# Kernel tuning notes

Measured on AMD Instinct MI355X. Metric: run time of the kernel, lower is better.

The kernel has to match this reference:

```python
import jax, jax.numpy as jnp
import numpy as np

NUM_RANGES = 31   # bins [0,1)...[29,30) plus [30, inf) -> max_height=30
EPS = 1e-06
ALPHA = 0.5
NAN_VALUE = -1.0


def setup_inputs() -> dict:
    key = jax.random.key(0)
    k1, k2 = jax.random.split(key)
    shape = (64, 512, 512)
    # targets in log1p space; natural heights expm1(target) span [0, ~34)
    target = jax.random.uniform(k1, shape, dtype=jnp.float32) * 3.55
    pred = target + 0.1 * jax.random.normal(k2, shape, dtype=jnp.float32)
    return {"pred": pred, "target": target}


def reference(pred, target):
    valid = target != NAN_VALUE                      # no-data mask
    natural = jnp.expm1(target)                      # heights in natural space
    # arithmetic bin index: ranges [i, i+1) for i<30, last bin [30, inf)
    bin_idx = jnp.clip(jnp.floor(natural), 0.0, NUM_RANGES - 1).astype(jnp.int32)
    in_range = natural >= 0.0                        # samples below 0 fall in no range

    # histogram of valid, in-range samples (scatter-add)
    counts = jnp.zeros(NUM_RANGES, jnp.float32).at[bin_idx.ravel()].add(
        (valid & in_range).ravel().astype(jnp.float32))
    total_valid = jnp.sum(valid).astype(jnp.float32)
    denom = jnp.maximum(total_valid, 1.0)
    freq = counts / denom
    w = 1.0 / (freq ** ALPHA + EPS)                  # inverse-frequency weights, [31]

    base = jnp.abs(pred - target)                    # L1 in log1p space
    sample_w = jnp.where(in_range, w[bin_idx], 0.0)  # gather per-sample weight
    weighted = base * sample_w
    # mean over valid samples (out-of-range valid samples contribute 0, as in torch)
    mean_loss = jnp.sum(jnp.where(valid, weighted, 0.0)) / denom
    return mean_loss
```

## Files before the change

kernel.cpp:

```cpp
#include <hip/hip_runtime.h>
#include <math.h>

#define NBINS 31
#define NSLOT 32
#define NCOPIES 256
#define BLOCK 256
#define GRID 512
#define DEPTH 4

#define CNT_SHIFT 24
#define SUM_MASK  0xFFFFFFu
#define FIX_SCALE 32768.0f

typedef float f4 __attribute__((ext_vector_type(4)));


__device__ __forceinline__ void prep(float p, float t, unsigned hbase,
                                     unsigned& addr, unsigned& pk, unsigned& nvalid)
{
    nvalid += (t != -1.0f) ? 1u : 0u;
    bool ok = (t >= 0.0f);
    float nat = __expf(t) - 1.0f;
    unsigned b = (unsigned)(int)fminf(nat, 30.0f);
    unsigned pkv = (1u << CNT_SHIFT)
                 | (unsigned)(fabsf(p - t) * FIX_SCALE + 0.5f);
    pk   = ok ? pkv : 0u;
    addr = hbase + ((ok ? b : 31u) << 10);
}

__device__ __forceinline__ void packet(f4 p, f4 t, unsigned hbase,
                                       unsigned& nvalid)
{
    unsigned a0, a1, a2, a3, k0, k1, k2, k3;
    prep(p.x, t.x, hbase, a0, k0, nvalid);
    prep(p.y, t.y, hbase, a1, k1, nvalid);
    prep(p.z, t.z, hbase, a2, k2, nvalid);
    prep(p.w, t.w, hbase, a3, k3, nvalid);

    unsigned r0, r1, r2, r3;
    asm volatile(
        "ds_read_b32 %0, %4\n\t"
        "ds_read_b32 %1, %5\n\t"
        "ds_read_b32 %2, %6\n\t"
        "ds_read_b32 %3, %7"
        : "=&v"(r0), "=&v"(r1), "=&v"(r2), "=&v"(r3)
        : "v"(a0), "v"(a1), "v"(a2), "v"(a3));

    unsigned s0 = k0;
    unsigned s1 = k1 + (a1 == a0 ? s0 : 0u);
    unsigned s2 = k2 + (a2 == a1 ? s1 : (a2 == a0 ? s0 : 0u));
    unsigned s3 = k3 + (a3 == a2 ? s2 : (a3 == a1 ? s1 : (a3 == a0 ? s0 : 0u)));

    asm volatile(
        "s_waitcnt lgkmcnt(0)\n\t"
        "v_add_u32 %0, %0, %4\n\t"
        "v_add_u32 %1, %1, %5\n\t"
        "v_add_u32 %2, %2, %6\n\t"
        "v_add_u32 %3, %3, %7\n\t"
        "ds_write_b32 %8, %0\n\t"
        "ds_write_b32 %9, %1\n\t"
        "ds_write_b32 %10, %2\n\t"
        "ds_write_b32 %11, %3"
        : "+v"(r0), "+v"(r1), "+v"(r2), "+v"(r3)
        : "v"(s0), "v"(s1), "v"(s2), "v"(s3),
          "v"(a0), "v"(a1), "v"(a2), "v"(a3));
}

__device__ __forceinline__ void stage(unsigned* dst, const f4* p4, const f4* t4,
                                      int idx)
{
    __builtin_amdgcn_global_load_lds(
        (const __attribute__((address_space(1))) unsigned*)(const void*)(p4 + idx),
        (__attribute__((address_space(3))) unsigned*)dst, 16, 0, 0);
    __builtin_amdgcn_global_load_lds(
        (const __attribute__((address_space(1))) unsigned*)(const void*)(t4 + idx),
        (__attribute__((address_space(3))) unsigned*)(dst + 256), 16, 0, 0);
}

__device__ __forceinline__ void unstage(unsigned sa, f4& pv, f4& tv)
{
    asm volatile(
        "ds_read_b128 %0, %2\n\t"
        "ds_read_b128 %1, %2 offset:1024\n\t"
        "s_waitcnt lgkmcnt(0)"
        : "=&v"(pv), "=&v"(tv)
        : "v"(sa));
}

__global__ __launch_bounds__(BLOCK) void zero_ws_kernel(unsigned* ws)
{
    int t = threadIdx.x;
    if (t < 192) ws[t] = 0u;
}

__global__ __launch_bounds__(BLOCK, 2) void hist_kernel(
    const float* __restrict__ pred, const float* __restrict__ target, int n,
    float* __restrict__ g_sums, unsigned* __restrict__ g_cnts,
    unsigned* __restrict__ g_total)
{
    __shared__ unsigned s_hist[NSLOT * NCOPIES];
    __shared__ unsigned s_stage[BLOCK / 64][DEPTH][512];
    __shared__ float    p_sum[NBINS * 8];
    __shared__ unsigned p_cnt[NBINS * 8];
    __shared__ unsigned s_tot[BLOCK / 64];

    const int tid = threadIdx.x;
    {
        uint4 z = make_uint4(0u, 0u, 0u, 0u);
        uint4* h4 = (uint4*)s_hist;
        #pragma unroll
        for (int k = 0; k < (NSLOT * NCOPIES / 4) / BLOCK; ++k) h4[tid + k * BLOCK] = z;
    }
    __syncthreads();

    const unsigned hbase = (unsigned)(uintptr_t)(void*)s_hist + ((unsigned)tid << 2);
    const int lane = tid & 63, wv = tid >> 6;
    unsigned* wb = &s_stage[wv][0][0];
    const unsigned sbase = (unsigned)(uintptr_t)(void*)wb + ((unsigned)lane << 4);
    unsigned nvalid = 0;

    const int n4 = n >> 2;
    const f4* __restrict__ pred4 = (const f4*)pred;
    const f4* __restrict__ targ4 = (const f4*)target;
    const int st = GRID * BLOCK;
    const int i0 = blockIdx.x * BLOCK + tid;
    const int T  = n4 / st;

    if ((n & 3) == 0 && (n4 % st) == 0 && T >= DEPTH) {
        stage(wb,        pred4, targ4, i0);
        stage(wb + 512,  pred4, targ4, i0 + st);
        stage(wb + 1024, pred4, targ4, i0 + 2 * st);
        int i = i0 + 3 * st;
        for (int k = 0; k < T; ++k, i += st) {
            if (k + 3 < T) {
                stage(wb + ((unsigned)((k + 3) & 3) << 9), pred4, targ4, i);
                asm volatile("s_waitcnt vmcnt(6)" ::: "memory");
            } else if (k + 2 < T) {
                asm volatile("s_waitcnt vmcnt(4)" ::: "memory");
            } else if (k + 1 < T) {
                asm volatile("s_waitcnt vmcnt(2)" ::: "memory");
            } else {
                asm volatile("s_waitcnt vmcnt(0)" ::: "memory");
            }
            f4 pv, tv;
            unstage(sbase + ((unsigned)(k & 3) << 11), pv, tv);
            packet(pv, tv, hbase, nvalid);
        }
    } else {
        for (int i = i0; i < n4; i += st) {
            f4 p = pred4[i];
            f4 t = targ4[i];
            packet(p, t, hbase, nvalid);
        }
        for (int i = (n4 << 2) + i0; i < n; i += st) {
            float p = pred[i], t = target[i];
            if (t != -1.0f) {
                atomicAdd(g_total, 1u);
                if (t >= 0.0f) {
                    float nat = __expf(t) - 1.0f;
                    int b = (int)fminf(nat, 30.0f);
                    atomicAdd(&g_sums[b], fabsf(p - t));
                    atomicAdd(&g_cnts[b], 1u);
                }
            }
        }
    }
    asm volatile("s_waitcnt lgkmcnt(0)" ::: "memory");
    __syncthreads();

    if (tid < NBINS * 8) {
        const int b = tid >> 3, g = tid & 7;
        const uint4* row = (const uint4*)(s_hist + b * NCOPIES);
        float fs = 0.0f; unsigned cs = 0u;
        #pragma unroll
        for (int kk = 0; kk < 8; ++kk) {
            uint4 v = row[g + 8 * kk];
            cs += (v.x >> CNT_SHIFT) + (v.y >> CNT_SHIFT)
                + (v.z >> CNT_SHIFT) + (v.w >> CNT_SHIFT);
            fs += (float)(v.x & SUM_MASK) + (float)(v.y & SUM_MASK)
                + (float)(v.z & SUM_MASK) + (float)(v.w & SUM_MASK);
        }
        p_sum[tid] = fs;
        p_cnt[tid] = cs;
    }
    unsigned v = nvalid;
    #pragma unroll
    for (int off = 32; off >= 1; off >>= 1) v += __shfl_down(v, off, 64);
    if ((tid & 63) == 0) s_tot[tid >> 6] = v;
    __syncthreads();

    if (tid < NBINS) {
        double fs = 0.0; unsigned cs = 0u;
        #pragma unroll
        for (int g = 0; g < 8; ++g) { fs += (double)p_sum[tid * 8 + g]; cs += p_cnt[tid * 8 + g]; }
        atomicAdd(&g_sums[tid], (float)(fs * (1.0 / (double)FIX_SCALE)));
        atomicAdd(&g_cnts[tid], cs);
    }
    if (tid == 0) {
        unsigned tot = 0;
        #pragma unroll
        for (int w = 0; w < BLOCK / 64; ++w) tot += s_tot[w];
        atomicAdd(g_total, tot);
    }
}

__global__ void finalize_kernel(const float* __restrict__ g_sums,
                                const unsigned* __restrict__ g_cnts,
                                const unsigned* __restrict__ g_total,
                                float* __restrict__ out)
{
    int lane = threadIdx.x;
    float denom = fmaxf((float)(*g_total), 1.0f);
    float contrib = 0.0f;
    if (lane < NBINS) {
        float freq = (float)g_cnts[lane] / denom;
        float w = 1.0f / (sqrtf(freq) + 1e-6f);
        contrib = g_sums[lane] * w;
    }
    #pragma unroll
    for (int off = 32; off >= 1; off >>= 1) contrib += __shfl_down(contrib, off, 64);
    if (lane == 0) *out = contrib / denom;
}

extern "C" void kernel_launch(void* const* d_in, const int* in_sizes, int n_in,
                              void* d_out, int out_size, void* d_ws, size_t ws_size,
                              hipStream_t stream)
{
    const float* pred   = (const float*)d_in[0];
    const float* target = (const float*)d_in[1];
    float* out = (float*)d_out;
    int n = in_sizes[0];

    float*    g_sums  = (float*)d_ws;
    unsigned* g_cnts  = (unsigned*)d_ws + 64;
    unsigned* g_total = (unsigned*)d_ws + 128;

    zero_ws_kernel<<<1, BLOCK, 0, stream>>>((unsigned*)d_ws);

    hist_kernel<<<GRID, BLOCK, 0, stream>>>(pred, target, n, g_sums, g_cnts, g_total);

    finalize_kernel<<<1, 64, 0, stream>>>(g_sums, g_cnts, g_total, out);
}
```

Before: 148.8 us.

## Replace LDS-staged prefetch with register-resident async global loads, double grid

Removes the global_load_lds staging buffers and instead issues inline-asm global_load_dwordx4 into a 4-deep register ring, waiting with explicit vmcnt counts before each histogram packet. This drops the LDS round trip (ds_read_b128) and frees LDS, which allows raising occupancy to 4 blocks per CU and doubling the grid to 1024 blocks. The risks are higher register pressure from 8 in-flight f4 loads, and reliance on the compiler not reordering around the asm waits. The fast path now also requires T divisible by 4.

After: 148.2 us. Within noise of the previous version (-0.4%).

```diff
diff --git a/kernel.cpp b/kernel.cpp
--- a/kernel.cpp
+++ b/kernel.cpp
@@ -5,12 +5,11 @@
 #define NSLOT 32
 #define NCOPIES 256
 #define BLOCK 256
-#define GRID 512
-#define DEPTH 4
-
+#define GRID 1024
 #define CNT_SHIFT 24
 #define SUM_MASK  0xFFFFFFu
 #define FIX_SCALE 32768.0f
+
 
 typedef float f4 __attribute__((ext_vector_type(4)));
 
@@ -66,40 +65,37 @@
           "v"(a0), "v"(a1), "v"(a2), "v"(a3));
 }
 
-__device__ __forceinline__ void stage(unsigned* dst, const f4* p4, const f4* t4,
-                                      int idx)
-{
-    __builtin_amdgcn_global_load_lds(
-        (const __attribute__((address_space(1))) unsigned*)(const void*)(p4 + idx),
-        (__attribute__((address_space(3))) unsigned*)dst, 16, 0, 0);
-    __builtin_amdgcn_global_load_lds(
-        (const __attribute__((address_space(1))) unsigned*)(const void*)(t4 + idx),
-        (__attribute__((address_space(3))) unsigned*)(dst + 256), 16, 0, 0);
-}
-
-__device__ __forceinline__ void unstage(unsigned sa, f4& pv, f4& tv)
-{
-    asm volatile(
-        "ds_read_b128 %0, %2\n\t"
-        "ds_read_b128 %1, %2 offset:1024\n\t"
-        "s_waitcnt lgkmcnt(0)"
-        : "=&v"(pv), "=&v"(tv)
-        : "v"(sa));
-}
-
 __global__ __launch_bounds__(BLOCK) void zero_ws_kernel(unsigned* ws)
 {
     int t = threadIdx.x;
     if (t < 192) ws[t] = 0u;
 }
 
-__global__ __launch_bounds__(BLOCK, 2) void hist_kernel(
+#define ISSUE(j) do {                                                      \
+    asm volatile("global_load_dwordx4 %0, %2, off\n\t"                     \
+                 "global_load_dwordx4 %1, %3, off"                         \
+                 : "=&v"(Sp[(j)]), "=&v"(St[(j)])                          \
+                 : "v"(ap), "v"(atg));                                     \
+    ap += stb; atg += stb; } while (0)
+
+#define WAITC(cnt, j)                                                      \
+    asm volatile("s_waitcnt vmcnt(" #cnt ")"                               \
+                 : "+v"(Sp[(j)]), "+v"(St[(j)]))
+
+#define PHASE(j) do {                                                      \
+    if (k + 3 < T)      { ISSUE((((j) + 3) & 3)); WAITC(6, (j)); }         \
+    else if (k + 2 < T) WAITC(4, (j));                                     \
+    else if (k + 1 < T) WAITC(2, (j));                                     \
+    else                WAITC(0, (j));                                     \
+    packet(Sp[(j)], St[(j)], hbase, nvalid);                               \
+    ++k; } while (0)
+
+__global__ __launch_bounds__(BLOCK, 4) void hist_kernel(
     const float* __restrict__ pred, const float* __restrict__ target, int n,
     float* __restrict__ g_sums, unsigned* __restrict__ g_cnts,
     unsigned* __restrict__ g_total)
 {
     __shared__ unsigned s_hist[NSLOT * NCOPIES];
-    __shared__ unsigned s_stage[BLOCK / 64][DEPTH][512];
     __shared__ float    p_sum[NBINS * 8];
     __shared__ unsigned p_cnt[NBINS * 8];
     __shared__ unsigned s_tot[BLOCK / 64];
@@ -114,9 +110,6 @@
     __syncthreads();
 
     const unsigned hbase = (unsigned)(uintptr_t)(void*)s_hist + ((unsigned)tid << 2);
-    const int lane = tid & 63, wv = tid >> 6;
-    unsigned* wb = &s_stage[wv][0][0];
-    const unsigned sbase = (unsigned)(uintptr_t)(void*)wb + ((unsigned)lane << 4);
     unsigned nvalid = 0;
 
     const int n4 = n >> 2;
@@ -126,26 +119,14 @@
     const int i0 = blockIdx.x * BLOCK + tid;
     const int T  = n4 / st;
 
-    if ((n & 3) == 0 && (n4 % st) == 0 && T >= DEPTH) {
-        stage(wb,        pred4, targ4, i0);
-        stage(wb + 512,  pred4, targ4, i0 + st);
-        stage(wb + 1024, pred4, targ4, i0 + 2 * st);
-        int i = i0 + 3 * st;
-        for (int k = 0; k < T; ++k, i += st) {
-            if (k + 3 < T) {
-                stage(wb + ((unsigned)((k + 3) & 3) << 9), pred4, targ4, i);
-                asm volatile("s_waitcnt vmcnt(6)" ::: "memory");
-            } else if (k + 2 < T) {
-                asm volatile("s_waitcnt vmcnt(4)" ::: "memory");
-            } else if (k + 1 < T) {
-                asm volatile("s_waitcnt vmcnt(2)" ::: "memory");
-            } else {
-                asm volatile("s_waitcnt vmcnt(0)" ::: "memory");
-            }
-            f4 pv, tv;
-            unstage(sbase + ((unsigned)(k & 3) << 11), pv, tv);
-            packet(pv, tv, hbase, nvalid);
-        }
+    if ((n & 3) == 0 && (n4 % st) == 0 && T >= 4 && (T & 3) == 0) {
+        unsigned long long ap  = (unsigned long long)(uintptr_t)(const void*)(pred4 + i0);
+        unsigned long long atg = (unsigned long long)(uintptr_t)(const void*)(targ4 + i0);
+        const unsigned long long stb = (unsigned long long)(unsigned)st * 16ull;
+        f4 Sp[4], St[4];
+        ISSUE(0); ISSUE(1); ISSUE(2);
+        int k = 0;
+        while (k < T) { PHASE(0); PHASE(1); PHASE(2); PHASE(3); }
     } else {
         for (int i = i0; i < n4; i += st) {
             f4 p = pred4[i];
```
